# Performance work log

Measured on AMD Instinct MI355X. Metric: run time of the kernel, lower is better.

## Reference

```python
import jax, jax.numpy as jnp
import numpy as np

B, H, T, D = 2, 16, 2048, 64
BASE_WINDOW = 256
FULL = 999999


def _make_window_sizes(num_heads=H, base_window=BASE_WINDOW):
    ws = []
    for h in range(num_heads):
        if h < num_heads // 4:
            ws.append(base_window)
        elif h < num_heads // 2:
            ws.append(base_window * 2)
        elif h < 3 * num_heads // 4:
            ws.append(base_window * 4)
        else:
            ws.append(FULL)
    return jnp.asarray(ws, dtype=jnp.int32)


def setup_inputs() -> dict:
    key = jax.random.key(0)
    kq, kk, kv = jax.random.split(key, 3)
    Q = jax.random.normal(kq, (B, H, T, D), dtype=jnp.float32)
    K = jax.random.normal(kk, (B, H, T, D), dtype=jnp.float32)
    V = jax.random.normal(kv, (B, H, T, D), dtype=jnp.float32)
    return {"Q": Q, "K": K, "V": V, "window_sizes": _make_window_sizes()}


def reference(Q, K, V, window_sizes):
    b, h, t, d = Q.shape
    scale = 1.0 / np.sqrt(d).astype(np.float32)
    idx = jnp.arange(t, dtype=jnp.int32)
    diff = idx[:, None] - idx[None, :]  # [T, T], q_idx - kv_idx
    # causal & |q-k| <= w  ==  0 <= diff <= w  (per head)
    mask = (diff >= 0) & (diff[None, :, :] <= window_sizes[:, None, None])  # [H, T, T]
    scores = jnp.einsum('bhqd,bhkd->bhqk', Q, K) * scale  # [B, H, T, T]
    scores = jnp.where(mask[None], scores, -jnp.inf)
    attn = jax.nn.softmax(scores, axis=-1)
    return jnp.einsum('bhqk,bhkd->bhqd', attn, V)
```

## Files before the change

### kernel.cpp

```cpp
#include <hip/hip_runtime.h>
#include <hip/hip_bf16.h>


constexpr int Bc = 2, Hc = 16, Tc = 2048, Dc = 64;
constexpr int BQ = 64;
constexpr int BK = 64;
constexpr int N_ITEMS = Bc * Hc * (Tc / BQ);
constexpr float QSCALE = 0.125f * 1.44269504088896340736f;
constexpr float CMAX = 16.0f;

constexpr size_t KB_OFF = 256;
constexpr size_t VB_OFF = 256 + (size_t)Bc * Hc * Tc * Dc * 2;
constexpr int HEADE = Tc * Dc;

constexpr int KOFF = 0;
constexpr int VOFF = 8192;
constexpr int POFF = 16384;

typedef __attribute__((ext_vector_type(8))) short short8;
typedef __attribute__((ext_vector_type(4))) float float4v;

#if defined(__has_builtin)
#if __has_builtin(__builtin_amdgcn_exp2f)
#define EXP2 __builtin_amdgcn_exp2f
#endif
#endif
#ifndef EXP2
#define EXP2 exp2f
#endif

__device__ inline unsigned f2bf_u(float f) {
    union { float f; unsigned u; } v; v.f = f;
    return (v.u + 0x7fffu + ((v.u >> 16) & 1u)) >> 16;
}

__device__ inline short8 pack8(const float* t) {
    short8 r;
#pragma unroll
    for (int j = 0; j < 8; j++) r[j] = (short)f2bf_u(t[j]);
    return r;
}

__device__ inline unsigned pk_bf16(float a, float b) {
    __hip_bfloat162 h = __float22bfloat162_rn(make_float2(a, b));
    union { __hip_bfloat162 h; unsigned u; } v; v.h = h;
    return v.u;
}

__device__ inline void dma16(const unsigned short* g, unsigned short* l) {
    __builtin_amdgcn_global_load_lds(
        (const __attribute__((address_space(1))) unsigned int*)g,
        (__attribute__((address_space(3))) unsigned int*)l, 16, 0, 0);
}

__global__ __launch_bounds__(256)
void preconv_kernel(const float* __restrict__ K, const float* __restrict__ V,
                    unsigned short* __restrict__ Kb, unsigned short* __restrict__ Vtb) {
    const int blk = blockIdx.x;
    const int tid = threadIdx.x;
    if (blk < 2048) {
        const int base = blk * 2048 + tid * 8;
        float4v a = *(const float4v*)(K + base);
        float4v b = *(const float4v*)(K + base + 4);
        float t[8] = {a[0], a[1], a[2], a[3], b[0], b[1], b[2], b[3]};
        *(short8*)(Kb + base) = pack8(t);
    } else {
        __shared__ float tile[64][65];
        const int blk2 = blk - 2048;
        const int bh = blk2 >> 5;
        const int t0 = (blk2 & 31) * 64;
        const float* src = V + (size_t)bh * HEADE + (size_t)t0 * Dc;
#pragma unroll
        for (int i = 0; i < 4; i++) {
            const int r = (tid >> 4) + i * 16;
            const int d4 = (tid & 15) * 4;
            float4v v4 = *(const float4v*)(src + r * Dc + d4);
            tile[r][d4] = v4[0]; tile[r][d4 + 1] = v4[1];
            tile[r][d4 + 2] = v4[2]; tile[r][d4 + 3] = v4[3];
        }
        __syncthreads();
        unsigned short* dst = Vtb + (size_t)bh * HEADE + t0;
#pragma unroll
        for (int i = 0; i < 2; i++) {
            const int d = (tid >> 3) + 32 * i;
            const int c = tid & 7;
            float t[8];
#pragma unroll
            for (int j = 0; j < 8; j++) t[j] = tile[c * 8 + j][d];
            *(short8*)(dst + (size_t)d * Tc + c * 8) = pack8(t);
        }
    }
}

__global__ __launch_bounds__(256, 4)
void dswa_kernel(const float* __restrict__ Q,
                 const unsigned short* __restrict__ Kb,
                 const unsigned short* __restrict__ Vtb,
                 const int* __restrict__ wsz,
                 float* __restrict__ O, unsigned* __restrict__ counter) {
    __shared__ __align__(16) unsigned short LDS[20480];

    const int tid  = threadIdx.x;
    const int wave = tid >> 6;
    const int g    = wave >> 1;
    const int wq   = wave & 1;
    const int lane = tid & 63;
    const int quad = lane >> 4;
    const int l16  = lane & 15;
    const int sw8  = (l16 & 7) << 3;

    unsigned short* Kl = &LDS[KOFF + g * 4096];
    unsigned short* Vt = &LDS[VOFF + g * 4096];
    unsigned short* Pl = &LDS[POFF + wave * 1024];
    int* ib = (int*)&LDS[POFF];

    const int lrow = lane >> 3;
    const int lcol = ((lane & 7) * 8) ^ ((lrow & 7) << 3);

    for (;;) {
        if (tid == 0) *ib = (int)atomicAdd(counter, 1u);
        __syncthreads();
        const int idx = *ib;
        if (idx >= N_ITEMS) break;

        const int b  = idx & 1;
        const int qt = 31 - ((idx >> 1) & 31);
        const int h  = 15 - (idx >> 6);
        const int q0 = qt * BQ;
        const int win = wsz[h];

        const size_t headoff = (size_t)(b * Hc + h) * HEADE;
        const float* Qp = Q + headoff;
        const unsigned short* Kbh = Kb + headoff;
        const unsigned short* Vbh = Vtb + headoff;
        float* Op = O + headoff;

        short8 qf[2][2];
#pragma unroll
        for (int s = 0; s < 2; s++) {
            const int qrow = q0 + wq * 32 + s * 16 + l16;
#pragma unroll
            for (int c = 0; c < 2; c++) {
                const float* src = Qp + (size_t)qrow * Dc + c * 32 + quad * 8;
                float4v a = *(const float4v*)src;
                float4v d4 = *(const float4v*)(src + 4);
                float t[8] = {a[0]*QSCALE, a[1]*QSCALE, a[2]*QSCALE, a[3]*QSCALE,
                              d4[0]*QSCALE, d4[1]*QSCALE, d4[2]*QSCALE, d4[3]*QSCALE};
                qf[s][c] = pack8(t);
            }
        }

        float4v acc[2][4];
#pragma unroll
        for (int s = 0; s < 2; s++)
#pragma unroll
            for (int nb = 0; nb < 4; nb++) acc[s][nb] = (float4v){0.f, 0.f, 0.f, 0.f};
        float lp0 = 0.0f, lp1 = 0.0f;

        const int kv_lo = (max(0, q0 - win)) & ~(BK - 1);
        const int n_tiles = (q0 + BQ - kv_lo) >> 6;
        const int IT = (n_tiles + 1) >> 1;

        const int kv0g = kv_lo + g * BK;
        const unsigned short* kgp = Kbh + (size_t)(kv0g + wq * 32 + lrow) * 64 + lcol;
        const unsigned short* vgp = Vbh + (size_t)(wq * 32 + lrow) * Tc + kv0g + lcol;

        for (int t = 0; t < IT; ++t) {
            const int ti = g + 2 * t;
            const bool act = ti < n_tiles;
            const int kv0 = kv_lo + ti * BK;

            __syncthreads();

            if (act) {
#pragma unroll
                for (int j = 0; j < 4; j++)
                    dma16(kgp + j * 512, &Kl[wq * 2048 + j * 512]);
#pragma unroll
                for (int j = 0; j < 4; j++)
                    dma16(vgp + (size_t)j * 8 * Tc, &Vt[wq * 2048 + j * 512]);
            }
            __asm__ volatile("" ::: "memory");
            __builtin_amdgcn_s_waitcnt(0x0f70);
            __asm__ volatile("" ::: "memory");
            __syncthreads();

            if (act) {
                float4v sT0[4], sT1[4];
#pragma unroll
                for (int mb = 0; mb < 4; mb++) {
                    float4v c0 = {-CMAX, -CMAX, -CMAX, -CMAX};
                    float4v c1 = {-CMAX, -CMAX, -CMAX, -CMAX};
#pragma unroll
                    for (int ch = 0; ch < 2; ch++) {
                        short8 kf = *(short8*)&Kl[(mb * 16 + l16) * 64 +
                                                  ((ch * 32 + quad * 8) ^ sw8)];
                        c0 = __builtin_amdgcn_mfma_f32_16x16x32_bf16(kf, qf[0][ch], c0, 0, 0, 0);
                        c1 = __builtin_amdgcn_mfma_f32_16x16x32_bf16(kf, qf[1][ch], c1, 0, 0, 0);
                    }
                    sT0[mb] = c0; sT1[mb] = c1;
                }

                short8 pf0[2], pf1[2];
                {
                    const int rs = q0 + wq * 32;
                    const bool interior = (rs >= kv0 + 63) && (rs + 15 - kv0 <= win);
                    if (!interior) {
                        const int dbase = rs + l16 - kv0 - quad * 4;
#pragma unroll
                        for (int mb = 0; mb < 4; mb++)
#pragma unroll
                            for (int r = 0; r < 4; r++) {
                                const unsigned diff = (unsigned)(dbase - mb * 16 - r);
                                sT0[mb][r] = (diff <= (unsigned)win) ? sT0[mb][r] : -3.0e38f;
                            }
                    }
#pragma unroll
                    for (int mb = 0; mb < 4; mb++) {
                        float p0 = EXP2(sT0[mb][0]);
                        float p1 = EXP2(sT0[mb][1]);
                        float p2 = EXP2(sT0[mb][2]);
                        float p3 = EXP2(sT0[mb][3]);
                        lp0 += (p0 + p1) + (p2 + p3);
                        unsigned* dst = (unsigned*)&Pl[l16 * 64 + ((mb * 16 + quad * 4) ^ sw8)];
                        dst[0] = pk_bf16(p0, p1);
                        dst[1] = pk_bf16(p2, p3);
                    }
                    __asm__ volatile("" ::: "memory");
#pragma unroll
                    for (int ch = 0; ch < 2; ch++)
                        pf0[ch] = *(short8*)&Pl[l16 * 64 + ((ch * 32 + quad * 8) ^ sw8)];
                }
                {
                    const int rs = q0 + wq * 32 + 16;
                    const bool interior = (rs >= kv0 + 63) && (rs + 15 - kv0 <= win);
                    if (!interior) {
                        const int dbase = rs + l16 - kv0 - quad * 4;
#pragma unroll
                        for (int mb = 0; mb < 4; mb++)
#pragma unroll
                            for (int r = 0; r < 4; r++) {
                                const unsigned diff = (unsigned)(dbase - mb * 16 - r);
                                sT1[mb][r] = (diff <= (unsigned)win) ? sT1[mb][r] : -3.0e38f;
                            }
                    }
                    __asm__ volatile("" ::: "memory");
#pragma unroll
                    for (int mb = 0; mb < 4; mb++) {
                        float p0 = EXP2(sT1[mb][0]);
                        float p1 = EXP2(sT1[mb][1]);
                        float p2 = EXP2(sT1[mb][2]);
                        float p3 = EXP2(sT1[mb][3]);
                        lp1 += (p0 + p1) + (p2 + p3);
                        unsigned* dst = (unsigned*)&Pl[l16 * 64 + ((mb * 16 + quad * 4) ^ sw8)];
                        dst[0] = pk_bf16(p0, p1);
                        dst[1] = pk_bf16(p2, p3);
                    }
                    __asm__ volatile("" ::: "memory");
#pragma unroll
                    for (int ch = 0; ch < 2; ch++)
                        pf1[ch] = *(short8*)&Pl[l16 * 64 + ((ch * 32 + quad * 8) ^ sw8)];
                }

#pragma unroll
                for (int nb = 0; nb < 4; nb++) {
#pragma unroll
                    for (int ch = 0; ch < 2; ch++) {
                        short8 vf = *(short8*)&Vt[(nb * 16 + l16) * 64 +
                                                  ((ch * 32 + quad * 8) ^ sw8)];
                        acc[0][nb] = __builtin_amdgcn_mfma_f32_16x16x32_bf16(pf0[ch], vf, acc[0][nb], 0, 0, 0);
                        acc[1][nb] = __builtin_amdgcn_mfma_f32_16x16x32_bf16(pf1[ch], vf, acc[1][nb], 0, 0, 0);
                    }
                }
            }
            kgp += 128 * 64;
            vgp += 128;
        }

        lp0 += __shfl_xor(lp0, 16); lp0 += __shfl_xor(lp0, 32);
        lp1 += __shfl_xor(lp1, 16); lp1 += __shfl_xor(lp1, 32);

        __syncthreads();
        float* fl = (float*)LDS;
        if (g == 1) {
#pragma unroll
            for (int s = 0; s < 2; s++) {
                if (quad == 0) fl[(wq * 32 + s * 16 + l16) * 66 + 64] = (s ? lp1 : lp0);
#pragma unroll
                for (int r = 0; r < 4; r++) {
                    const int row = wq * 32 + s * 16 + quad * 4 + r;
#pragma unroll
                    for (int nb = 0; nb < 4; nb++)
                        fl[row * 66 + nb * 16 + l16] = acc[s][nb][r];
                }
            }
        }
        __syncthreads();
        if (g == 0) {
#pragma unroll
            for (int s = 0; s < 2; s++) {
                const float lps = s ? lp1 : lp0;
#pragma unroll
                for (int r = 0; r < 4; r++) {
                    const int row = wq * 32 + s * 16 + quad * 4 + r;
                    const float l0 = __shfl(lps, quad * 4 + r);
                    const float lt = l0 + fl[row * 66 + 64];
                    const float inv = 1.0f / lt;
                    float* dst = Op + (size_t)(q0 + row) * Dc;
#pragma unroll
                    for (int nb = 0; nb < 4; nb++)
                        dst[nb * 16 + l16] = (acc[s][nb][r] + fl[row * 66 + nb * 16 + l16]) * inv;
                }
            }
        }
    }
}

extern "C" void kernel_launch(void* const* d_in, const int* in_sizes, int n_in,
                              void* d_out, int out_size, void* d_ws, size_t ws_size,
                              hipStream_t stream) {
    (void)in_sizes; (void)n_in; (void)ws_size; (void)out_size;
    const float* Q = (const float*)d_in[0];
    const float* K = (const float*)d_in[1];
    const float* V = (const float*)d_in[2];
    const int* wsz = (const int*)d_in[3];
    float* Out = (float*)d_out;

    unsigned* counter = (unsigned*)d_ws;
    unsigned short* Kb  = (unsigned short*)((char*)d_ws + KB_OFF);
    unsigned short* Vtb = (unsigned short*)((char*)d_ws + VB_OFF);

    hipMemsetAsync(counter, 0, sizeof(unsigned), stream);
    preconv_kernel<<<dim3(3072), dim3(256), 0, stream>>>(K, V, Kb, Vtb);
    dswa_kernel<<<dim3(1024), dim3(256), 0, stream>>>(Q, Kb, Vtb, wsz, Out, counter);
}
```

Baseline: 141.6 us.

## Replace persistent atomic scheduler with static blocks and register-prefetched double-buffered KV tiles

Drops the atomic work-counter persistent loop and its memset in favour of one block per (b,h,q-tile), mapped statically with heavy heads first. The KV tile shrinks from 64 to 32 keys per group, and global_load_lds DMA is replaced by register prefetch of the next tile into double-buffered LDS, with a padded V layout. This cuts the per-iteration barriers to one and overlaps global loads with compute. In exchange it loses dynamic load balancing across the uneven windows and issues twice as many smaller tiles.

```diff
diff --git a/kernel.cpp b/kernel.cpp
--- a/kernel.cpp
+++ b/kernel.cpp
@@ -4,8 +4,7 @@
 
 constexpr int Bc = 2, Hc = 16, Tc = 2048, Dc = 64;
 constexpr int BQ = 64;
-constexpr int BK = 64;
-constexpr int N_ITEMS = Bc * Hc * (Tc / BQ);
+constexpr int BK = 32;
 constexpr float QSCALE = 0.125f * 1.44269504088896340736f;
 constexpr float CMAX = 16.0f;
 
@@ -15,7 +14,7 @@
 
 constexpr int KOFF = 0;
 constexpr int VOFF = 8192;
-constexpr int POFF = 16384;
+constexpr int POFF = 18432;
 
 typedef __attribute__((ext_vector_type(8))) short short8;
 typedef __attribute__((ext_vector_type(4))) float float4v;
@@ -45,12 +44,6 @@
     __hip_bfloat162 h = __float22bfloat162_rn(make_float2(a, b));
     union { __hip_bfloat162 h; unsigned u; } v; v.h = h;
     return v.u;
-}
-
-__device__ inline void dma16(const unsigned short* g, unsigned short* l) {
-    __builtin_amdgcn_global_load_lds(
-        (const __attribute__((address_space(1))) unsigned int*)g,
-        (__attribute__((address_space(3))) unsigned int*)l, 16, 0, 0);
 }
 
 __global__ __launch_bounds__(256)
@@ -97,7 +90,7 @@
                  const unsigned short* __restrict__ Kb,
                  const unsigned short* __restrict__ Vtb,
                  const int* __restrict__ wsz,
-                 float* __restrict__ O, unsigned* __restrict__ counter) {
+                 float* __restrict__ O) {
     __shared__ __align__(16) unsigned short LDS[20480];
 
     const int tid  = threadIdx.x;
@@ -107,210 +100,211 @@
     const int lane = tid & 63;
     const int quad = lane >> 4;
     const int l16  = lane & 15;
-    const int sw8  = (l16 & 7) << 3;
-
-    unsigned short* Kl = &LDS[KOFF + g * 4096];
-    unsigned short* Vt = &LDS[VOFF + g * 4096];
-    unsigned short* Pl = &LDS[POFF + wave * 1024];
-    int* ib = (int*)&LDS[POFF];
-
-    const int lrow = lane >> 3;
-    const int lcol = ((lane & 7) * 8) ^ ((lrow & 7) << 3);
-
-    for (;;) {
-        if (tid == 0) *ib = (int)atomicAdd(counter, 1u);
+    const int ksw  = 0;  (void)ksw;
+    const int psw  = (l16 & 3) << 3;
+
+    unsigned short* Kg = &LDS[KOFF + g * 4096];
+    unsigned short* Vg = &LDS[VOFF + g * 5120];
+    unsigned short* Pl = &LDS[POFF + wave * 512];
+
+    const int l128 = tid & 127;
+    const int krow = l128 >> 2;
+    const int kcol = (l128 & 3) * 16;
+    const int vrow = l128 >> 1;
+    const int vcol = (l128 & 1) * 16;
+
+    const int blk = blockIdx.x;
+    const int b  = blk & 1;
+    const int qt = 31 - ((blk >> 1) & 31);
+    const int h  = 15 - (blk >> 6);
+    const int q0 = qt * BQ;
+    const int win = wsz[h];
+
+    const size_t headoff = (size_t)(b * Hc + h) * HEADE;
+    const float* Qp = Q + headoff;
+    const unsigned short* Kbh = Kb + headoff;
+    const unsigned short* Vbh = Vtb + headoff;
+    float* Op = O + headoff;
+
+    short8 qf[2][2];
+#pragma unroll
+    for (int s = 0; s < 2; s++) {
+        const int qrow = q0 + wq * 32 + s * 16 + l16;
+#pragma unroll
+        for (int c = 0; c < 2; c++) {
+            const float* src = Qp + (size_t)qrow * Dc + c * 32 + quad * 8;
+            float4v a = *(const float4v*)src;
+            float4v d4 = *(const float4v*)(src + 4);
+            float t[8] = {a[0]*QSCALE, a[1]*QSCALE, a[2]*QSCALE, a[3]*QSCALE,
+                          d4[0]*QSCALE, d4[1]*QSCALE, d4[2]*QSCALE, d4[3]*QSCALE};
+            qf[s][c] = pack8(t);
+        }
+    }
+
+    float4v acc[2][4];
+#pragma unroll
+    for (int s = 0; s < 2; s++)
+#pragma unroll
+        for (int nb = 0; nb < 4; nb++) acc[s][nb] = (float4v){0.f, 0.f, 0.f, 0.f};
+    float lp0 = 0.0f, lp1 = 0.0f;
+
+    const int kv_lo = (max(0, q0 - win)) & ~(BK - 1);
+    const int n_tiles = (q0 + BQ - kv_lo) >> 5;
+    const int IT = (n_tiles + 1) >> 1;
+
+    const int kv0g = kv_lo + g * BK;
+    const unsigned short* kgp = Kbh + (size_t)(kv0g + krow) * Dc + kcol;
+    const unsigned short* vgp = Vbh + (size_t)vrow * Tc + kv0g + vcol;
+
+    short8 kr0, kr1, vr0, vr1;
+    if (g < n_tiles) {
+        kr0 = *(const short8*)(kgp);
+        kr1 = *(const short8*)(kgp + 8);
+        vr0 = *(const short8*)(vgp);
+        vr1 = *(const short8*)(vgp + 8);
+    }
+    kgp += 64 * Dc; vgp += 64;
+
+    for (int t = 0; t < IT; ++t) {
+        const int ti = g + 2 * t;
+        const bool act = ti < n_tiles;
+        const int kv0 = kv_lo + ti * BK;
+        unsigned short* Kl = Kg + (t & 1) * 2048;
+        unsigned short* Vt = Vg + (t & 1) * 2560;
+
+        if (act) {
+            const int ks = (krow & 7) << 3;
+            *(short8*)&Kl[krow * 64 + (kcol ^ ks)] = kr0;
+            *(short8*)&Kl[krow * 64 + ((kcol + 8) ^ ks)] = kr1;
+            *(short8*)&Vt[vrow * 40 + vcol] = vr0;
+            *(short8*)&Vt[vrow * 40 + vcol + 8] = vr1;
+        }
         __syncthreads();
-        const int idx = *ib;
-        if (idx >= N_ITEMS) break;
-
-        const int b  = idx & 1;
-        const int qt = 31 - ((idx >> 1) & 31);
-        const int h  = 15 - (idx >> 6);
-        const int q0 = qt * BQ;
-        const int win = wsz[h];
-
-        const size_t headoff = (size_t)(b * Hc + h) * HEADE;
-        const float* Qp = Q + headoff;
-        const unsigned short* Kbh = Kb + headoff;
-        const unsigned short* Vbh = Vtb + headoff;
-        float* Op = O + headoff;
-
-        short8 qf[2][2];
+
+        if (ti + 2 < n_tiles) {
+            kr0 = *(const short8*)(kgp);
+            kr1 = *(const short8*)(kgp + 8);
+            vr0 = *(const short8*)(vgp);
+            vr1 = *(const short8*)(vgp + 8);
+        }
+        kgp += 64 * Dc; vgp += 64;
+
+        if (act) {
+            float4v sT0[2], sT1[2];
+#pragma unroll
+            for (int mb = 0; mb < 2; mb++) {
+                float4v c0 = {-CMAX, -CMAX, -CMAX, -CMAX};
+                float4v c1 = {-CMAX, -CMAX, -CMAX, -CMAX};
+#pragma unroll
+                for (int ch = 0; ch < 2; ch++) {
+                    const int row = mb * 16 + l16;
+                    short8 kf = *(short8*)&Kl[row * 64 +
+                                              ((ch * 32 + quad * 8) ^ ((row & 7) << 3))];
+                    c0 = __builtin_amdgcn_mfma_f32_16x16x32_bf16(kf, qf[0][ch], c0, 0, 0, 0);
+                    c1 = __builtin_amdgcn_mfma_f32_16x16x32_bf16(kf, qf[1][ch], c1, 0, 0, 0);
+                }
+                sT0[mb] = c0; sT1[mb] = c1;
+            }
+
+            short8 pf0, pf1;
+            {
+                const int rs = q0 + wq * 32;
+                const bool interior = (kv0 + 31 <= rs) && (rs + 15 - kv0 <= win);
+                if (!interior) {
+                    const int dbase = rs + l16 - kv0 - quad * 4;
+#pragma unroll
+                    for (int mb = 0; mb < 2; mb++)
+#pragma unroll
+                        for (int r = 0; r < 4; r++) {
+                            const unsigned diff = (unsigned)(dbase - mb * 16 - r);
+                            sT0[mb][r] = (diff <= (unsigned)win) ? sT0[mb][r] : -3.0e38f;
+                        }
+                }
+#pragma unroll
+                for (int mb = 0; mb < 2; mb++) {
+                    float p0 = EXP2(sT0[mb][0]);
+                    float p1 = EXP2(sT0[mb][1]);
+                    float p2 = EXP2(sT0[mb][2]);
+                    float p3 = EXP2(sT0[mb][3]);
+                    lp0 += (p0 + p1) + (p2 + p3);
+                    unsigned* dst = (unsigned*)&Pl[l16 * 32 + ((mb * 16 + quad * 4) ^ psw)];
+                    dst[0] = pk_bf16(p0, p1);
+                    dst[1] = pk_bf16(p2, p3);
+                }
+                __asm__ volatile("" ::: "memory");
+                pf0 = *(short8*)&Pl[l16 * 32 + ((quad * 8) ^ psw)];
+            }
+            {
+                const int rs = q0 + wq * 32 + 16;
+                const bool interior = (kv0 + 31 <= rs) && (rs + 15 - kv0 <= win);
+                if (!interior) {
+                    const int dbase = rs + l16 - kv0 - quad * 4;
+#pragma unroll
+                    for (int mb = 0; mb < 2; mb++)
+#pragma unroll
+                        for (int r = 0; r < 4; r++) {
+                            const unsigned diff = (unsigned)(dbase - mb * 16 - r);
+                            sT1[mb][r] = (diff <= (unsigned)win) ? sT1[mb][r] : -3.0e38f;
+                        }
+                }
+                __asm__ volatile("" ::: "memory");
+#pragma unroll
+                for (int mb = 0; mb < 2; mb++) {
+                    float p0 = EXP2(sT1[mb][0]);
+                    float p1 = EXP2(sT1[mb][1]);
+                    float p2 = EXP2(sT1[mb][2]);
+                    float p3 = EXP2(sT1[mb][3]);
+                    lp1 += (p0 + p1) + (p2 + p3);
+                    unsigned* dst = (unsigned*)&Pl[l16 * 32 + ((mb * 16 + quad * 4) ^ psw)];
+                    dst[0] = pk_bf16(p0, p1);
+                    dst[1] = pk_bf16(p2, p3);
+                }
+                __asm__ volatile("" ::: "memory");
+                pf1 = *(short8*)&Pl[l16 * 32 + ((quad * 8) ^ psw)];
+            }
+
+#pragma unroll
+            for (int nb = 0; nb < 4; nb++) {
+                short8 vf = *(short8*)&Vt[(nb * 16 + l16) * 40 + quad * 8];
+                acc[0][nb] = __builtin_amdgcn_mfma_f32_16x16x32_bf16(pf0, vf, acc[0][nb], 0, 0, 0);
+                acc[1][nb] = __builtin_amdgcn_mfma_f32_16x16x32_bf16(pf1, vf, acc[1][nb], 0, 0, 0);
+            }
+        }
+    }
+
+    lp0 += __shfl_xor(lp0, 16); lp0 += __shfl_xor(lp0, 32);
+    lp1 += __shfl_xor(lp1, 16); lp1 += __shfl_xor(lp1, 32);
+
+    __syncthreads();
+    float* fl = (float*)LDS;
+    if (g == 1) {
 #pragma unroll
         for (int s = 0; s < 2; s++) {
-            const int qrow = q0 + wq * 32 + s * 16 + l16;
-#pragma unroll
-            for (int c = 0; c < 2; c++) {
-                const float* src = Qp + (size_t)qrow * Dc + c * 32 + quad * 8;
-                float4v a = *(const float4v*)src;
-                float4v d4 = *(const float4v*)(src + 4);
-                float t[8] = {a[0]*QSCALE, a[1]*QSCALE, a[2]*QSCALE, a[3]*QSCALE,
-                              d4[0]*QSCALE, d4[1]*QSCALE, d4[2]*QSCALE, d4[3]*QSCALE};
-                qf[s][c] = pack8(t);
-            }
-        }
-
-        float4v acc[2][4];
-#pragma unroll
-        for (int s = 0; s < 2; s++)
-#pragma unroll
-            for (int nb = 0; nb < 4; nb++) acc[s][nb] = (float4v){0.f, 0.f, 0.f, 0.f};
-        float lp0 = 0.0f, lp1 = 0.0f;
-
-        const int kv_lo = (max(0, q0 - win)) & ~(BK - 1);
-        const int n_tiles = (q0 + BQ - kv_lo) >> 6;
-        const int IT = (n_tiles + 1) >> 1;
-
-        const int kv0g = kv_lo + g * BK;
-        const unsigned short* kgp = Kbh + (size_t)(kv0g + wq * 32 + lrow) * 64 + lcol;
-        const unsigned short* vgp = Vbh + (size_t)(wq * 32 + lrow) * Tc + kv0g + lcol;
-
-        for (int t = 0; t < IT; ++t) {
-            const int ti = g + 2 * t;
-            const bool act = ti < n_tiles;
-            const int kv0 = kv_lo + ti * BK;
-
-            __syncthreads();
-
-            if (act) {
-#pragma unroll
-                for (int j = 0; j < 4; j++)
-                    dma16(kgp + j * 512, &Kl[wq * 2048 + j * 512]);
-#pragma unroll
-                for (int j = 0; j < 4; j++)
-                    dma16(vgp + (size_t)j * 8 * Tc, &Vt[wq * 2048 + j * 512]);
-            }
-            __asm__ volatile("" ::: "memory");
-            __builtin_amdgcn_s_waitcnt(0x0f70);
-            __asm__ volatile("" ::: "memory");
-            __syncthreads();
-
-            if (act) {
-                float4v sT0[4], sT1[4];
-#pragma unroll
-                for (int mb = 0; mb < 4; mb++) {
-                    float4v c0 = {-CMAX, -CMAX, -CMAX, -CMAX};
-                    float4v c1 = {-CMAX, -CMAX, -CMAX, -CMAX};
-#pragma unroll
-                    for (int ch = 0; ch < 2; ch++) {
-                        short8 kf = *(short8*)&Kl[(mb * 16 + l16) * 64 +
-                                                  ((ch * 32 + quad * 8) ^ sw8)];
-                        c0 = __builtin_amdgcn_mfma_f32_16x16x32_bf16(kf, qf[0][ch], c0, 0, 0, 0);
-                        c1 = __builtin_amdgcn_mfma_f32_16x16x32_bf16(kf, qf[1][ch], c1, 0, 0, 0);
-                    }
-                    sT0[mb] = c0; sT1[mb] = c1;
-                }
-
-                short8 pf0[2], pf1[2];
-                {
-                    const int rs = q0 + wq * 32;
-                    const bool interior = (rs >= kv0 + 63) && (rs + 15 - kv0 <= win);
-                    if (!interior) {
-                        const int dbase = rs + l16 - kv0 - quad * 4;
-#pragma unroll
-                        for (int mb = 0; mb < 4; mb++)
-#pragma unroll
-                            for (int r = 0; r < 4; r++) {
-                                const unsigned diff = (unsigned)(dbase - mb * 16 - r);
-                                sT0[mb][r] = (diff <= (unsigned)win) ? sT0[mb][r] : -3.0e38f;
-                            }
-                    }
-#pragma unroll
-                    for (int mb = 0; mb < 4; mb++) {
-                        float p0 = EXP2(sT0[mb][0]);
-                        float p1 = EXP2(sT0[mb][1]);
-                        float p2 = EXP2(sT0[mb][2]);
-                        float p3 = EXP2(sT0[mb][3]);
-                        lp0 += (p0 + p1) + (p2 + p3);
-                        unsigned* dst = (unsigned*)&Pl[l16 * 64 + ((mb * 16 + quad * 4) ^ sw8)];
-                        dst[0] = pk_bf16(p0, p1);
-                        dst[1] = pk_bf16(p2, p3);
-                    }
-                    __asm__ volatile("" ::: "memory");
-#pragma unroll
-                    for (int ch = 0; ch < 2; ch++)
-                        pf0[ch] = *(short8*)&Pl[l16 * 64 + ((ch * 32 + quad * 8) ^ sw8)];
-                }
-                {
-                    const int rs = q0 + wq * 32 + 16;
-                    const bool interior = (rs >= kv0 + 63) && (rs + 15 - kv0 <= win);
-                    if (!interior) {
-                        const int dbase = rs + l16 - kv0 - quad * 4;
-#pragma unroll
-                        for (int mb = 0; mb < 4; mb++)
-#pragma unroll
-                            for (int r = 0; r < 4; r++) {
-                                const unsigned diff = (unsigned)(dbase - mb * 16 - r);
-                                sT1[mb][r] = (diff <= (unsigned)win) ? sT1[mb][r] : -3.0e38f;
-                            }
-                    }
-                    __asm__ volatile("" ::: "memory");
-#pragma unroll
-                    for (int mb = 0; mb < 4; mb++) {
-                        float p0 = EXP2(sT1[mb][0]);
-                        float p1 = EXP2(sT1[mb][1]);
-                        float p2 = EXP2(sT1[mb][2]);
-                        float p3 = EXP2(sT1[mb][3]);
-                        lp1 += (p0 + p1) + (p2 + p3);
-                        unsigned* dst = (unsigned*)&Pl[l16 * 64 + ((mb * 16 + quad * 4) ^ sw8)];
-                        dst[0] = pk_bf16(p0, p1);
-                        dst[1] = pk_bf16(p2, p3);
-                    }
-                    __asm__ volatile("" ::: "memory");
-#pragma unroll
-                    for (int ch = 0; ch < 2; ch++)
-                        pf1[ch] = *(short8*)&Pl[l16 * 64 + ((ch * 32 + quad * 8) ^ sw8)];
-                }
-
-#pragma unroll
-                for (int nb = 0; nb < 4; nb++) {
-#pragma unroll
-                    for (int ch = 0; ch < 2; ch++) {
-                        short8 vf = *(short8*)&Vt[(nb * 16 + l16) * 64 +
-                                                  ((ch * 32 + quad * 8) ^ sw8)];
-                        acc[0][nb] = __builtin_amdgcn_mfma_f32_16x16x32_bf16(pf0[ch], vf, acc[0][nb], 0, 0, 0);
-                        acc[1][nb] = __builtin_amdgcn_mfma_f32_16x16x32_bf16(pf1[ch], vf, acc[1][nb], 0, 0, 0);
-                    }
-                }
-            }
-            kgp += 128 * 64;
-            vgp += 128;
-        }
-
-        lp0 += __shfl_xor(lp0, 16); lp0 += __shfl_xor(lp0, 32);
-        lp1 += __shfl_xor(lp1, 16); lp1 += __shfl_xor(lp1, 32);
-
-        __syncthreads();
-        float* fl = (float*)LDS;
-        if (g == 1) {
-#pragma unroll
-            for (int s = 0; s < 2; s++) {
-                if (quad == 0) fl[(wq * 32 + s * 16 + l16) * 66 + 64] = (s ? lp1 : lp0);
-#pragma unroll
-                for (int r = 0; r < 4; r++) {
-                    const int row = wq * 32 + s * 16 + quad * 4 + r;
-#pragma unroll
-                    for (int nb = 0; nb < 4; nb++)
-                        fl[row * 66 + nb * 16 + l16] = acc[s][nb][r];
-                }
-            }
-        }
-        __syncthreads();
-        if (g == 0) {
-#pragma unroll
-            for (int s = 0; s < 2; s++) {
-                const float lps = s ? lp1 : lp0;
-#pragma unroll
-                for (int r = 0; r < 4; r++) {
-                    const int row = wq * 32 + s * 16 + quad * 4 + r;
-                    const float l0 = __shfl(lps, quad * 4 + r);
-                    const float lt = l0 + fl[row * 66 + 64];
-                    const float inv = 1.0f / lt;
-                    float* dst = Op + (size_t)(q0 + row) * Dc;
-#pragma unroll
-                    for (int nb = 0; nb < 4; nb++)
-                        dst[nb * 16 + l16] = (acc[s][nb][r] + fl[row * 66 + nb * 16 + l16]) * inv;
-                }
+            if (quad == 0) fl[(wq * 32 + s * 16 + l16) * 66 + 64] = (s ? lp1 : lp0);
+#pragma unroll
+            for (int r = 0; r < 4; r++) {
+                const int row = wq * 32 + s * 16 + quad * 4 + r;
+#pragma unroll
+                for (int nb = 0; nb < 4; nb++)
+                    fl[row * 66 + nb * 16 + l16] = acc[s][nb][r];
+            }
+        }
+    }
+    __syncthreads();
+    if (g == 0) {
+#pragma unroll
+        for (int s = 0; s < 2; s++) {
+            const float lps = s ? lp1 : lp0;
+#pragma unroll
+            for (int r = 0; r < 4; r++) {
+                const int row = wq * 32 + s * 16 + quad * 4 + r;
+                const float l0 = __shfl(lps, quad * 4 + r);
+                const float lt = l0 + fl[row * 66 + 64];
+                const float inv = 1.0f / lt;
+                float* dst = Op + (size_t)(q0 + row) * Dc;
+#pragma unroll
+                for (int nb = 0; nb < 4; nb++)
+                    dst[nb * 16 + l16] = (acc[s][nb][r] + fl[row * 66 + nb * 16 + l16]) * inv;
             }
         }
     }
@@ -326,11 +320,9 @@
     const int* wsz = (const int*)d_in[3];
     float* Out = (float*)d_out;
 
-    unsigned* counter = (unsigned*)d_ws;
     unsigned short* Kb  = (unsigned short*)((char*)d_ws + KB_OFF);
     unsigned short* Vtb = (unsigned short*)((char*)d_ws + VB_OFF);
 
-    hipMemsetAsync(counter, 0, sizeof(unsigned), stream);
     preconv_kernel<<<dim3(3072), dim3(256), 0, stream>>>(K, V, Kb, Vtb);
-    dswa_kernel<<<dim3(1024), dim3(256), 0, stream>>>(Q, Kb, Vtb, wsz, Out, counter);
-}
+    dswa_kernel<<<dim3(1024), dim3(256), 0, stream>>>(Q, Kb, Vtb, wsz, Out);
+}
```

Measured after the change: 125.7 us. 11.2% less time.
